# Optimization experiments

Measured on AMD Instinct MI355X. Metric: run time of the kernel, lower is better.

Reference implementation:

```python
import jax, jax.numpy as jnp
import numpy as np

DIM = 1024
NUM_HEADS = 16
HEAD_DIM = DIM // NUM_HEADS
SCALE = HEAD_DIM ** (-0.5)
B, N = 2, 2048


def setup_inputs() -> dict:
    key = jax.random.key(0)
    ks = jax.random.split(key, 9)
    s = DIM ** (-0.5)
    return {
        "x": jax.random.normal(ks[0], (B, N, DIM), dtype=jnp.float32),
        "Wq": jax.random.normal(ks[1], (DIM, DIM), dtype=jnp.float32) * s,
        "bq": jax.random.normal(ks[2], (DIM,), dtype=jnp.float32) * 0.01,
        "Wk": jax.random.normal(ks[3], (DIM, DIM), dtype=jnp.float32) * s,
        "bk": jax.random.normal(ks[4], (DIM,), dtype=jnp.float32) * 0.01,
        "Wv": jax.random.normal(ks[5], (DIM, DIM), dtype=jnp.float32) * s,
        "bv": jax.random.normal(ks[6], (DIM,), dtype=jnp.float32) * 0.01,
        "Wp": jax.random.normal(ks[7], (DIM, DIM), dtype=jnp.float32) * s,
        "bp": jax.random.normal(ks[8], (DIM,), dtype=jnp.float32) * 0.01,
    }


def reference(x, Wq, bq, Wk, bk, Wv, bv, Wp, bp):
    Bb, Nn, C = x.shape
    # Linear layers (torch Linear: x @ W.T + b)
    q = x @ Wq.T + bq
    k = x @ Wk.T + bk
    v = x @ Wv.T + bv
    # [B, H, N, Dh]
    q = q.reshape(Bb, Nn, NUM_HEADS, HEAD_DIM).transpose(0, 2, 1, 3) * SCALE
    k = k.reshape(Bb, Nn, NUM_HEADS, HEAD_DIM).transpose(0, 2, 1, 3)
    v = v.reshape(Bb, Nn, NUM_HEADS, HEAD_DIM).transpose(0, 2, 1, 3)
    # float32 scores (original casts q,k to float before matmul)
    attn = jnp.einsum("bhnd,bhmd->bhnm", q.astype(jnp.float32), k.astype(jnp.float32))
    attn = jax.nn.softmax(attn, axis=-1).astype(x.dtype)
    out = jnp.einsum("bhnm,bhmd->bhnd", attn, v)
    out = out.transpose(0, 2, 1, 3).reshape(Bb, Nn, C)
    return out @ Wp.T + bp
```

## Files before the change

### kernel.cpp

```cpp
#include <hip/hip_runtime.h>
#include <hip/hip_bf16.h>
#include <stdint.h>

#define SEQ   2048
#define NDIM  1024
#define NH    16
#define DH    64
#define NB    2
#define MROWS (NB*SEQ)
#define S2SCALE (0.125f * 1.44269504f)

typedef __attribute__((ext_vector_type(8))) short bf16x8;
typedef __attribute__((ext_vector_type(4))) float f32x4;


__device__ __forceinline__ unsigned short f2bf(float f) {
  union { float f; unsigned int u; } v; v.f = f;
  unsigned int u = v.u;
  return (unsigned short)((u + 0x7fffu + ((u >> 16) & 1u)) >> 16);
}

__device__ __forceinline__ unsigned int cvtpk(float a, float b) {
  unsigned int r;
  asm("v_cvt_pk_bf16_f32 %0, %1, %2" : "=v"(r) : "v"(a), "v"(b));
  return r;
}

__device__ __forceinline__ float exp2fast(float x) {
#if __has_builtin(__builtin_amdgcn_exp2f)
  return __builtin_amdgcn_exp2f(x);
#else
  float r; asm volatile("v_exp_f32 %0, %1" : "=v"(r) : "v"(x)); return r;
#endif
}

__device__ __forceinline__ void pl32swap(unsigned int& x, unsigned int& y) {
  asm("v_permlane32_swap_b32 %0, %1" : "+v"(x), "+v"(y));
}
__device__ __forceinline__ void pl16swap(unsigned int& x, unsigned int& y) {
  asm("v_permlane16_swap_b32 %0, %1" : "+v"(x), "+v"(y));
}

__device__ __forceinline__ void drain_vmem() {
  asm volatile("s_waitcnt vmcnt(0)" ::: "memory");
  __builtin_amdgcn_sched_barrier(0);
}

__device__ __forceinline__ void gld16(const void* g, void* l) {
  __builtin_amdgcn_global_load_lds(
      (const __attribute__((address_space(1))) void*)g,
      (__attribute__((address_space(3))) void*)l,
      16, 0, 0);
}

__global__ __launch_bounds__(256) void cvt_all(
    const float* __restrict__ x,  const float* __restrict__ wq,
    const float* __restrict__ wk, const float* __restrict__ wv,
    const float* __restrict__ wp,
    unsigned short* __restrict__ xb,  unsigned short* __restrict__ wqb,
    unsigned short* __restrict__ wkb, unsigned short* __restrict__ wvb,
    unsigned short* __restrict__ wpb)
{
  int c = blockIdx.x * 256 + threadIdx.x;
  const float* s; unsigned short* d;
  if (c < (MROWS*NDIM/8)) { s = x; d = xb; }
  else {
    c -= MROWS*NDIM/8;
    int w = c >> 17; c &= (1<<17)-1;
    s = (w==0)?wq:(w==1)?wk:(w==2)?wv:wp;
    d = (w==0)?wqb:(w==1)?wkb:(w==2)?wvb:wpb;
  }
  size_t off = (size_t)c * 8;
  const float4* sp = (const float4*)(s + off);
  float4 a = sp[0], b4 = sp[1];
  unsigned int u0 = (unsigned)f2bf(a.x)  | ((unsigned)f2bf(a.y)  << 16);
  unsigned int u1 = (unsigned)f2bf(a.z)  | ((unsigned)f2bf(a.w)  << 16);
  unsigned int u2 = (unsigned)f2bf(b4.x) | ((unsigned)f2bf(b4.y) << 16);
  unsigned int u3 = (unsigned)f2bf(b4.z) | ((unsigned)f2bf(b4.w) << 16);
  uint4 o; o.x = u0; o.y = u1; o.z = u2; o.w = u3;
  *(uint4*)(d + off) = o;
}

template<int BM>
__device__ __forceinline__ void gemm_loop(
    const unsigned short* __restrict__ A0,
    const unsigned short* __restrict__ B0,
    int K, f32x4 (&acc)[BM/32][4], char* ldsA, char* ldsB)
{
  constexpr int MI   = BM/32;
  constexpr int APIT = BM/32;
  const int tid = threadIdx.x;
  const int lane = tid & 63, g = lane >> 4, l15 = lane & 15;
  const int wv = tid >> 6, wm = wv >> 1, wn = wv & 1;

  int srowA[APIT], scolA[APIT], srowB[4], scolB[4];
#pragma unroll
  for (int p = 0; p < APIT; ++p) {
    int idx = p*256 + tid;
    int row = idx >> 3, c = idx & 7;
    srowA[p] = row;
    scolA[p] = (c ^ (row & 7)) * 8;
  }
#pragma unroll
  for (int p = 0; p < 4; ++p) {
    int idx = p*256 + tid;
    int row = idx >> 3, c = idx & 7;
    srowB[p] = row;
    scolB[p] = (c ^ (row & 7)) * 8;
  }
  int offA[MI][2], offB[4][2];
#pragma unroll
  for (int f = 0; f < MI; ++f) {
    int ra = wm*(BM/2) + f*16 + l15;
#pragma unroll
    for (int kc = 0; kc < 2; ++kc)
      offA[f][kc] = ra*128 + (((kc*4 + g) ^ (ra & 7)) * 16);
  }
#pragma unroll
  for (int f = 0; f < 4; ++f) {
    int rb = wn*64 + f*16 + l15;
#pragma unroll
    for (int kc = 0; kc < 2; ++kc)
      offB[f][kc] = rb*128 + (((kc*4 + g) ^ (rb & 7)) * 16);
  }

  for (int k0 = 0; k0 < K; k0 += 64) {
#pragma unroll
    for (int p = 0; p < APIT; ++p)
      gld16(A0 + (size_t)srowA[p]*K + k0 + scolA[p], ldsA + p*4096 + wv*1024);
#pragma unroll
    for (int p = 0; p < 4; ++p)
      gld16(B0 + (size_t)srowB[p]*K + k0 + scolB[p], ldsB + p*4096 + wv*1024);
    drain_vmem();
    __syncthreads();
    bf16x8 af[MI][2], bfr[4][2];
#pragma unroll
    for (int f = 0; f < MI; ++f)
#pragma unroll
      for (int kc = 0; kc < 2; ++kc) af[f][kc] = *(const bf16x8*)(ldsA + offA[f][kc]);
#pragma unroll
    for (int f = 0; f < 4; ++f)
#pragma unroll
      for (int kc = 0; kc < 2; ++kc) bfr[f][kc] = *(const bf16x8*)(ldsB + offB[f][kc]);
#pragma unroll
    for (int kc = 0; kc < 2; ++kc)
#pragma unroll
      for (int i = 0; i < MI; ++i)
#pragma unroll
        for (int j = 0; j < 4; ++j)
          acc[i][j] = __builtin_amdgcn_mfma_f32_16x16x32_bf16(af[i][kc], bfr[j][kc], acc[i][j], 0, 0, 0);
    __syncthreads();
  }
}

__global__ __launch_bounds__(256, 3) void gemm_qkv(
    const unsigned short* __restrict__ xb,
    const unsigned short* __restrict__ wqb, const unsigned short* __restrict__ wkb,
    const unsigned short* __restrict__ wvb,
    const float* __restrict__ bq, const float* __restrict__ bk, const float* __restrict__ bv,
    unsigned short* __restrict__ qb, unsigned short* __restrict__ kb,
    unsigned short* __restrict__ vtb)
{
  __shared__ __align__(16) char lds[32768];
  const int z = blockIdx.z;
  const unsigned short* W = (z==0)?wqb:(z==1)?wkb:wvb;
  const float* bias = (z==0)?bq:(z==1)?bk:bv;
  const int n0 = blockIdx.x * 128, m0 = blockIdx.y * 128;

  f32x4 acc[4][4];
#pragma unroll
  for (int i = 0; i < 4; ++i)
#pragma unroll
    for (int j = 0; j < 4; ++j) acc[i][j] = (f32x4){0.f, 0.f, 0.f, 0.f};

  gemm_loop<128>(xb + (size_t)m0*NDIM, W + (size_t)n0*NDIM, NDIM, acc, lds, lds + 16384);

  const int lane = threadIdx.x & 63, g = lane >> 4, l15 = lane & 15;
  const int wvx = threadIdx.x >> 6, wm = wvx >> 1, wn = wvx & 1;

  if (z < 2) {
    unsigned short* out = (z==0) ? qb : kb;
    const float sc = (z==0) ? S2SCALE : 1.0f;
#pragma unroll
    for (int i = 0; i < 4; ++i)
#pragma unroll
      for (int j = 0; j < 4; ++j) {
        int col = n0 + wn*64 + j*16 + l15;
        float bb = bias[col];
#pragma unroll
        for (int r = 0; r < 4; ++r) {
          int row = m0 + wm*64 + i*16 + g*4 + r;
          out[(size_t)row*NDIM + col] = f2bf((acc[i][j][r] + bb) * sc);
        }
      }
  } else {
#pragma unroll
    for (int i = 0; i < 4; ++i)
#pragma unroll
      for (int j = 0; j < 4; ++j) {
        int col = n0 + wn*64 + j*16 + l15;
        float bb = bias[col];
        int row0 = m0 + wm*64 + i*16 + g*4;
        int b_ = row0 >> 11, n_ = row0 & (SEQ-1);
        unsigned long long pk =
            (unsigned long long)f2bf(acc[i][j][0] + bb)
          | ((unsigned long long)f2bf(acc[i][j][1] + bb) << 16)
          | ((unsigned long long)f2bf(acc[i][j][2] + bb) << 32)
          | ((unsigned long long)f2bf(acc[i][j][3] + bb) << 48);
        *(unsigned long long*)(vtb + ((size_t)(b_*NDIM + col))*SEQ + n_) = pk;
      }
  }
}

__global__ __launch_bounds__(256, 2) void attn_fwd(
    const unsigned short* __restrict__ qb, const unsigned short* __restrict__ kb,
    const unsigned short* __restrict__ vtb, unsigned short* __restrict__ ob)
{
  __shared__ __align__(16) char lds[32768];
  const int tid = threadIdx.x, lane = tid & 63, g = lane >> 4, l15 = lane & 15;
  const int wvx = tid >> 6;
  const int bh = blockIdx.y, b_ = bh >> 4, h = bh & 15;
  const int qbase = blockIdx.x*128 + wvx*32;

  int srow[2], scol[2];
#pragma unroll
  for (int p = 0; p < 2; ++p) {
    int idx = p*256 + tid;
    int row = idx >> 3, c = idx & 7;
    srow[p] = row;
    scol[p] = (c ^ (row & 7)) * 8;
  }

  bf16x8 qf[2][2];
#pragma unroll
  for (int fn = 0; fn < 2; ++fn) {
    size_t row = (size_t)(b_*SEQ + qbase + fn*16 + l15);
#pragma unroll
    for (int kc = 0; kc < 2; ++kc)
      qf[fn][kc] = *(const bf16x8*)(qb + row*NDIM + h*DH + kc*32 + g*8);
  }

  float lacc[2] = {0.f, 0.f};
  f32x4 o_[2][4];
#pragma unroll
  for (int fn = 0; fn < 2; ++fn)
#pragma unroll
    for (int fd = 0; fd < 4; ++fd) o_[fn][fd] = (f32x4){0.f, 0.f, 0.f, 0.f};

#pragma unroll
  for (int p = 0; p < 2; ++p) {
    gld16(kb  + ((size_t)(b_*SEQ + srow[p]))*NDIM + h*DH + scol[p],
          lds + p*4096 + wvx*1024);
    gld16(vtb + ((size_t)(b_*NDIM + h*DH + srow[p]))*SEQ + scol[p],
          lds + 8192 + p*4096 + wvx*1024);
  }
  drain_vmem();
  __syncthreads();

  int cur = 0;
  for (int t = 0; t < SEQ/64; ++t) {
    if (t < SEQ/64 - 1) {
      const int k0n = (t+1)*64;
      char* Kd = lds + (cur^1)*16384;
#pragma unroll
      for (int p = 0; p < 2; ++p) {
        gld16(kb  + ((size_t)(b_*SEQ + k0n + srow[p]))*NDIM + h*DH + scol[p],
              Kd + p*4096 + wvx*1024);
        gld16(vtb + ((size_t)(b_*NDIM + h*DH + srow[p]))*SEQ + k0n + scol[p],
              Kd + 8192 + p*4096 + wvx*1024);
      }
    }
    char* Ks = lds + cur*16384;
    char* Vs = Ks + 8192;

    bf16x8 kf[4][2];
#pragma unroll
    for (int fm = 0; fm < 4; ++fm)
#pragma unroll
      for (int kc = 0; kc < 2; ++kc) {
        int row = fm*16 + l15;
        kf[fm][kc] = *(const bf16x8*)(Ks + row*128 + (((kc*4+g) ^ (row & 7))*16));
      }

    f32x4 st[2][4];
#pragma unroll
    for (int fn = 0; fn < 2; ++fn)
#pragma unroll
      for (int fm = 0; fm < 4; ++fm) st[fn][fm] = (f32x4){0.f, 0.f, 0.f, 0.f};
    __builtin_amdgcn_s_setprio(1);
#pragma unroll
    for (int kc = 0; kc < 2; ++kc)
#pragma unroll
      for (int fn = 0; fn < 2; ++fn)
#pragma unroll
        for (int fm = 0; fm < 4; ++fm)
          st[fn][fm] = __builtin_amdgcn_mfma_f32_16x16x32_bf16(kf[fm][kc], qf[fn][kc], st[fn][fm], 0, 0, 0);
    __builtin_amdgcn_s_setprio(0);

    bf16x8 pf[2][2];
#pragma unroll
    for (int fn = 0; fn < 2; ++fn) {
      unsigned int w[4][2];
#pragma unroll
      for (int fm = 0; fm < 4; ++fm) {
        float p0 = exp2fast(st[fn][fm][0]);
        float p1 = exp2fast(st[fn][fm][1]);
        float p2 = exp2fast(st[fn][fm][2]);
        float p3 = exp2fast(st[fn][fm][3]);
        lacc[fn] += (p0 + p1) + (p2 + p3);
        w[fm][0] = cvtpk(p0, p1);
        w[fm][1] = cvtpk(p2, p3);
      }
#pragma unroll
      for (int kc = 0; kc < 2; ++kc) {
        unsigned int x0 = w[kc*2][0], y0 = w[kc*2+1][0];
        pl32swap(x0, y0); pl16swap(x0, y0);
        unsigned int x1 = w[kc*2][1], y1 = w[kc*2+1][1];
        pl32swap(x1, y1); pl16swap(x1, y1);
        union { unsigned int u[4]; bf16x8 v; } uu;
        uu.u[0] = x0; uu.u[1] = x1; uu.u[2] = y0; uu.u[3] = y1;
        pf[fn][kc] = uu.v;
      }
    }

    bf16x8 vf[4][2];
#pragma unroll
    for (int fd = 0; fd < 4; ++fd)
#pragma unroll
      for (int ks = 0; ks < 2; ++ks) {
        int row = fd*16 + l15;
        vf[fd][ks] = *(const bf16x8*)(Vs + row*128 + (((ks*4+g) ^ (row & 7))*16));
      }
    __builtin_amdgcn_s_setprio(1);
#pragma unroll
    for (int ks = 0; ks < 2; ++ks)
#pragma unroll
      for (int fn = 0; fn < 2; ++fn)
#pragma unroll
        for (int fd = 0; fd < 4; ++fd)
          o_[fn][fd] = __builtin_amdgcn_mfma_f32_16x16x32_bf16(vf[fd][ks], pf[fn][ks], o_[fn][fd], 0, 0, 0);
    __builtin_amdgcn_s_setprio(0);

    drain_vmem();
    __syncthreads();
    cur ^= 1;
  }

#pragma unroll
  for (int fn = 0; fn < 2; ++fn) {
    float l = lacc[fn];
    l += __shfl_xor(l, 16);
    l += __shfl_xor(l, 32);
    float inv = 1.f / l;
    size_t row = (size_t)(b_*SEQ + qbase + fn*16 + l15);
#pragma unroll
    for (int fd = 0; fd < 4; ++fd) {
      unsigned long long pk =
          (unsigned long long)f2bf(o_[fn][fd][0]*inv)
        | ((unsigned long long)f2bf(o_[fn][fd][1]*inv) << 16)
        | ((unsigned long long)f2bf(o_[fn][fd][2]*inv) << 32)
        | ((unsigned long long)f2bf(o_[fn][fd][3]*inv) << 48);
      *(unsigned long long*)(ob + row*NDIM + h*DH + fd*16 + g*4) = pk;
    }
  }
}

__global__ __launch_bounds__(256, 2) void gemm_proj(
    const unsigned short* __restrict__ ob, const unsigned short* __restrict__ wpb,
    const float* __restrict__ bp, float* __restrict__ out)
{
  __shared__ __align__(16) char lds[24576];
  const int n0 = blockIdx.x * 128, m0 = blockIdx.y * 64;
  f32x4 acc[2][4];
#pragma unroll
  for (int i = 0; i < 2; ++i)
#pragma unroll
    for (int j = 0; j < 4; ++j) acc[i][j] = (f32x4){0.f, 0.f, 0.f, 0.f};

  gemm_loop<64>(ob + (size_t)m0*NDIM, wpb + (size_t)n0*NDIM, NDIM, acc, lds, lds + 8192);

  const int lane = threadIdx.x & 63, g = lane >> 4, l15 = lane & 15;
  const int wvx = threadIdx.x >> 6, wm = wvx >> 1, wn = wvx & 1;
#pragma unroll
  for (int i = 0; i < 2; ++i)
#pragma unroll
    for (int j = 0; j < 4; ++j) {
      int col = n0 + wn*64 + j*16 + l15;
      float bb = bp[col];
#pragma unroll
      for (int r = 0; r < 4; ++r) {
        int row = m0 + wm*32 + i*16 + g*4 + r;
        out[(size_t)row*NDIM + col] = acc[i][j][r] + bb;
      }
    }
}

extern "C" void kernel_launch(void* const* d_in, const int* in_sizes, int n_in,
                              void* d_out, int out_size, void* d_ws, size_t ws_size,
                              hipStream_t stream) {
  const float* x  = (const float*)d_in[0];
  const float* Wq = (const float*)d_in[1];
  const float* bq = (const float*)d_in[2];
  const float* Wk = (const float*)d_in[3];
  const float* bk = (const float*)d_in[4];
  const float* Wv = (const float*)d_in[5];
  const float* bv = (const float*)d_in[6];
  const float* Wp = (const float*)d_in[7];
  const float* bp = (const float*)d_in[8];
  float* out = (float*)d_out;

  char* ws = (char*)d_ws;
  const size_t MB = (size_t)1 << 20;
  unsigned short* xb  = (unsigned short*)(ws + 0*MB);
  unsigned short* wqb = (unsigned short*)(ws + 8*MB);
  unsigned short* wkb = (unsigned short*)(ws + 10*MB);
  unsigned short* wvb = (unsigned short*)(ws + 12*MB);
  unsigned short* wpb = (unsigned short*)(ws + 14*MB);
  unsigned short* qb  = (unsigned short*)(ws + 16*MB);
  unsigned short* kb  = (unsigned short*)(ws + 24*MB);
  unsigned short* vtb = (unsigned short*)(ws + 32*MB);
  unsigned short* ob  = (unsigned short*)(ws + 40*MB);

  hipLaunchKernelGGL(cvt_all, dim3(4096), dim3(256), 0, stream,
                     x, Wq, Wk, Wv, Wp, xb, wqb, wkb, wvb, wpb);
  hipLaunchKernelGGL(gemm_qkv, dim3(NDIM/128, MROWS/128, 3), dim3(256), 0, stream,
                     xb, wqb, wkb, wvb, bq, bk, bv, qb, kb, vtb);
  hipLaunchKernelGGL(attn_fwd, dim3(SEQ/128, NB*NH), dim3(256), 0, stream,
                     qb, kb, vtb, ob);
  hipLaunchKernelGGL(gemm_proj, dim3(NDIM/128, MROWS/64), dim3(256), 0, stream,
                     ob, wpb, bp, out);
}
```

Before: 178.7 us.

## Double-buffer LDS in QKV and projection GEMM loops to overlap loads

Turns the shared GEMM main loop into a two-stage ping-pong pipeline. The next K tile is loaded asynchronously into the alternate LDS buffer while MFMAs run on the current one, which hides global-load latency and drops one barrier per iteration. LDS usage doubles, so the QKV kernel's launch bound falls from three to two blocks per CU, which may cut occupancy.

```diff
diff --git a/kernel.cpp b/kernel.cpp
--- a/kernel.cpp
+++ b/kernel.cpp
@@ -82,13 +82,15 @@
 }
 
 template<int BM>
-__device__ __forceinline__ void gemm_loop(
+__device__ __forceinline__ void gemm_loop_db(
     const unsigned short* __restrict__ A0,
     const unsigned short* __restrict__ B0,
-    int K, f32x4 (&acc)[BM/32][4], char* ldsA, char* ldsB)
+    int K, f32x4 (&acc)[BM/32][4], char* lds)
 {
-  constexpr int MI   = BM/32;
-  constexpr int APIT = BM/32;
+  constexpr int MI     = BM/32;
+  constexpr int APIT   = BM/32;
+  constexpr int ABYTES = BM*128;
+  constexpr int BUF    = ABYTES + 16384;
   const int tid = threadIdx.x;
   const int lane = tid & 63, g = lane >> 4, l15 = lane & 15;
   const int wv = tid >> 6, wm = wv >> 1, wn = wv & 1;
@@ -124,36 +126,53 @@
       offB[f][kc] = rb*128 + (((kc*4 + g) ^ (rb & 7)) * 16);
   }
 
+  {
+    char* ldsA = lds; char* ldsB = lds + ABYTES;
+#pragma unroll
+    for (int p = 0; p < APIT; ++p)
+      gld16(A0 + (size_t)srowA[p]*K + scolA[p], ldsA + p*4096 + wv*1024);
+#pragma unroll
+    for (int p = 0; p < 4; ++p)
+      gld16(B0 + (size_t)srowB[p]*K + scolB[p], ldsB + p*4096 + wv*1024);
+  }
+  drain_vmem();
+  __syncthreads();
+
+  int cur = 0;
   for (int k0 = 0; k0 < K; k0 += 64) {
-#pragma unroll
-    for (int p = 0; p < APIT; ++p)
-      gld16(A0 + (size_t)srowA[p]*K + k0 + scolA[p], ldsA + p*4096 + wv*1024);
-#pragma unroll
-    for (int p = 0; p < 4; ++p)
-      gld16(B0 + (size_t)srowB[p]*K + k0 + scolB[p], ldsB + p*4096 + wv*1024);
+    if (k0 + 64 < K) {
+      char* ldsA = lds + (cur^1)*BUF; char* ldsB = ldsA + ABYTES;
+#pragma unroll
+      for (int p = 0; p < APIT; ++p)
+        gld16(A0 + (size_t)srowA[p]*K + (k0+64) + scolA[p], ldsA + p*4096 + wv*1024);
+#pragma unroll
+      for (int p = 0; p < 4; ++p)
+        gld16(B0 + (size_t)srowB[p]*K + (k0+64) + scolB[p], ldsB + p*4096 + wv*1024);
+    }
+    char* ldsA = lds + cur*BUF; char* ldsB = ldsA + ABYTES;
+    bf16x8 af[MI][2], bfr[4][2];
+#pragma unroll
+    for (int f = 0; f < MI; ++f)
+#pragma unroll
+      for (int kc = 0; kc < 2; ++kc) af[f][kc] = *(const bf16x8*)(ldsA + offA[f][kc]);
+#pragma unroll
+    for (int f = 0; f < 4; ++f)
+#pragma unroll
+      for (int kc = 0; kc < 2; ++kc) bfr[f][kc] = *(const bf16x8*)(ldsB + offB[f][kc]);
+#pragma unroll
+    for (int kc = 0; kc < 2; ++kc)
+#pragma unroll
+      for (int i = 0; i < MI; ++i)
+#pragma unroll
+        for (int j = 0; j < 4; ++j)
+          acc[i][j] = __builtin_amdgcn_mfma_f32_16x16x32_bf16(af[i][kc], bfr[j][kc], acc[i][j], 0, 0, 0);
     drain_vmem();
     __syncthreads();
-    bf16x8 af[MI][2], bfr[4][2];
-#pragma unroll
-    for (int f = 0; f < MI; ++f)
-#pragma unroll
-      for (int kc = 0; kc < 2; ++kc) af[f][kc] = *(const bf16x8*)(ldsA + offA[f][kc]);
-#pragma unroll
-    for (int f = 0; f < 4; ++f)
-#pragma unroll
-      for (int kc = 0; kc < 2; ++kc) bfr[f][kc] = *(const bf16x8*)(ldsB + offB[f][kc]);
-#pragma unroll
-    for (int kc = 0; kc < 2; ++kc)
-#pragma unroll
-      for (int i = 0; i < MI; ++i)
-#pragma unroll
-        for (int j = 0; j < 4; ++j)
-          acc[i][j] = __builtin_amdgcn_mfma_f32_16x16x32_bf16(af[i][kc], bfr[j][kc], acc[i][j], 0, 0, 0);
-    __syncthreads();
-  }
-}
-
-__global__ __launch_bounds__(256, 3) void gemm_qkv(
+    cur ^= 1;
+  }
+}
+
+__global__ __launch_bounds__(256, 2) void gemm_qkv(
     const unsigned short* __restrict__ xb,
     const unsigned short* __restrict__ wqb, const unsigned short* __restrict__ wkb,
     const unsigned short* __restrict__ wvb,
@@ -161,7 +180,7 @@
     unsigned short* __restrict__ qb, unsigned short* __restrict__ kb,
     unsigned short* __restrict__ vtb)
 {
-  __shared__ __align__(16) char lds[32768];
+  __shared__ __align__(16) char lds[65536];
   const int z = blockIdx.z;
   const unsigned short* W = (z==0)?wqb:(z==1)?wkb:wvb;
   const float* bias = (z==0)?bq:(z==1)?bk:bv;
@@ -173,7 +192,7 @@
 #pragma unroll
     for (int j = 0; j < 4; ++j) acc[i][j] = (f32x4){0.f, 0.f, 0.f, 0.f};
 
-  gemm_loop<128>(xb + (size_t)m0*NDIM, W + (size_t)n0*NDIM, NDIM, acc, lds, lds + 16384);
+  gemm_loop_db<128>(xb + (size_t)m0*NDIM, W + (size_t)n0*NDIM, NDIM, acc, lds);
 
   const int lane = threadIdx.x & 63, g = lane >> 4, l15 = lane & 15;
   const int wvx = threadIdx.x >> 6, wm = wvx >> 1, wn = wvx & 1;
@@ -369,7 +388,7 @@
     const unsigned short* __restrict__ ob, const unsigned short* __restrict__ wpb,
     const float* __restrict__ bp, float* __restrict__ out)
 {
-  __shared__ __align__(16) char lds[24576];
+  __shared__ __align__(16) char lds[49152];
   const int n0 = blockIdx.x * 128, m0 = blockIdx.y * 64;
   f32x4 acc[2][4];
 #pragma unroll
@@ -377,7 +396,7 @@
 #pragma unroll
     for (int j = 0; j < 4; ++j) acc[i][j] = (f32x4){0.f, 0.f, 0.f, 0.f};
 
-  gemm_loop<64>(ob + (size_t)m0*NDIM, wpb + (size_t)n0*NDIM, NDIM, acc, lds, lds + 8192);
+  gemm_loop_db<64>(ob + (size_t)m0*NDIM, wpb + (size_t)n0*NDIM, NDIM, acc, lds);
 
   const int lane = threadIdx.x & 63, g = lane >> 4, l15 = lane & 15;
   const int wvx = threadIdx.x >> 6, wm = wvx >> 1, wn = wvx & 1;
```

New measurement: 186.9 us. 1.05x slower.
